# Performance work log

Hardware: AMD Instinct MI355X
Metric: run time of the kernel (lower is better)

Reference implementation:

```python
import jax, jax.numpy as jnp
import numpy as np
from jax.ops import segment_sum

N = 50000        # nodes
E = 800000       # edges (avg degree 16)
H = 128          # hidden_dim
N_ITER = 2       # BCRefinement n_iterations
TIE_P = 0.05     # fraction of tie (boundary) edges


def setup_inputs() -> dict:
    key = jax.random.key(0)
    ks = jax.random.split(key, 24)
    s = 0.02
    inp = {
        'h': jax.random.normal(ks[0], (N, H), jnp.float32),
        'e': jax.random.normal(ks[1], (E, H), jnp.float32),
        'edge_attr_raw': jax.random.normal(ks[2], (E, 10), jnp.float32),
        # edge_refine: Linear(3H,2H) -> ReLU -> Linear(2H,H)
        'W_er1': s * jax.random.normal(ks[3], (3 * H, 2 * H), jnp.float32),
        'b_er1': jnp.zeros((2 * H,), jnp.float32),
        'W_er2': s * jax.random.normal(ks[4], (2 * H, H), jnp.float32),
        'b_er2': jnp.zeros((H,), jnp.float32),
        # GRUCell(H,H) torch layout: [3H, H] chunks (r, z, n)
        'W_ih': s * jax.random.normal(ks[5], (3 * H, H), jnp.float32),
        'W_hh': s * jax.random.normal(ks[6], (3 * H, H), jnp.float32),
        'b_ih': jnp.zeros((3 * H,), jnp.float32),
        'b_hh': jnp.zeros((3 * H,), jnp.float32),
        # node_neigh_fc: Linear(H,H)
        'W_nn': s * jax.random.normal(ks[7], (H, H), jnp.float32),
        'b_nn': jnp.zeros((H,), jnp.float32),
        # gate_mlp: Linear(3H,H) -> ReLU -> Linear(H,1), last bias init -2.0
        'W_g1': s * jax.random.normal(ks[8], (3 * H, H), jnp.float32),
        'b_g1': jnp.zeros((H,), jnp.float32),
        'W_g2': s * jax.random.normal(ks[9], (H, 1), jnp.float32),
        'b_g2': jnp.full((1,), -2.0, jnp.float32),
        'edge_index': jax.random.randint(ks[10], (2, E), 0, N, jnp.int32),
        'is_tie': jax.random.uniform(ks[11], (E,)) < TIE_P,
    }
    return inp


def reference(h, e, edge_attr_raw,
              W_er1, b_er1, W_er2, b_er2,
              W_ih, W_hh, b_ih, b_hh,
              W_nn, b_nn,
              W_g1, b_g1, W_g2, b_g2,
              edge_index, is_tie):
    row = edge_index[0]
    col = edge_index[1]
    tie_f = is_tie.astype(h.dtype)                        # [E]
    internal = ~is_tie

    # coupling buses: endpoints of any tie edge (tie-incidence count > 0)
    cpl_cnt = segment_sum(tie_f, row, num_segments=N) + \
              segment_sum(tie_f, col, num_segments=N)     # [N]
    is_cpl = cpl_cnt > 0

    # internal edges pointing into coupling buses; b_smooth weights w = 1/sqrt(X^2+eps)
    to_cpl = internal & is_cpl[col]
    X = jnp.abs(edge_attr_raw[:, 1])
    w = jnp.where(to_cpl, 1.0 / jnp.sqrt(X * X + 1e-6), 0.0)
    w_den = segment_sum(w, col, num_segments=N)           # [N]
    w_norm = w / (w_den[col] + 1e-6)                      # [E], zero off-mask

    deg = jnp.maximum(cpl_cnt, 1.0)                       # clamp_min(1.0)

    h_work, e_work = h, e
    for _ in range(N_ITER):
        # --- tie-edge refinement (applied only on tie edges) ---
        edge_in = jnp.concatenate([e_work, h_work[row], h_work[col]], axis=-1)  # [E,3H]
        e_ref = jax.nn.relu(edge_in @ W_er1 + b_er1) @ W_er2 + b_er2            # [E,H]
        e_work = e_work + tie_f[:, None] * e_ref

        # --- node messages from internal neighbors into coupling buses ---
        m_node_msg = h_work[row] @ W_nn + b_nn                                   # [E,H]
        m_node_all = segment_sum(m_node_msg * w_norm[:, None], col,
                                 num_segments=N)                                 # [N,H]

        # --- mean of incident tie-edge features at each node ---
        tie_e = tie_f[:, None] * e_work                                          # [E,H]
        m_edge_all = (segment_sum(tie_e, row, num_segments=N) +
                      segment_sum(tie_e, col, num_segments=N)) / deg[:, None]    # [N,H]

        # --- gating + GRU update on coupling buses ---
        gate_in = jnp.concatenate([m_edge_all, m_node_all, h_work], axis=-1)     # [N,3H]
        gate = jax.nn.sigmoid(jax.nn.relu(gate_in @ W_g1 + b_g1) @ W_g2 + b_g2)  # [N,1]
        m = m_edge_all + gate * m_node_all                                       # [N,H]

        gi = m @ W_ih.T + b_ih                                                   # [N,3H]
        gh = h_work @ W_hh.T + b_hh
        r = jax.nn.sigmoid(gi[:, :H] + gh[:, :H])
        z = jax.nn.sigmoid(gi[:, H:2 * H] + gh[:, H:2 * H])
        n = jnp.tanh(gi[:, 2 * H:] + r * gh[:, 2 * H:])
        h_new = (1.0 - z) * n + z * h_work

        h_work = jnp.where(is_cpl[:, None], h_new, h_work)
    return h_work, e_work
```

## Files before the change

kernel.cpp:

```cpp
#include <hip/hip_runtime.h>
#include <cstdint>

#define N_NODES 50000
#define N_EDGES 800000
#define HDIM    128
#define TIE_CAP 44000
#define NITER   2
#define SCAN_B  256
#define EB_CONST 3125
#define TB_CONST 172
#define GM_T     344
#define COPY_B   1664

typedef __attribute__((ext_vector_type(8))) short bf16x8;
typedef __attribute__((ext_vector_type(4))) float f32x4;

__device__ __forceinline__ uint32_t f2bf(float f) {
    uint32_t u = __builtin_bit_cast(uint32_t, f);
    return (u + 0x7fffu + ((u >> 16) & 1u)) >> 16;
}
__device__ __forceinline__ float bf2f(uint32_t b) {
    return __builtin_bit_cast(float, b << 16);
}
__device__ __forceinline__ uint32_t comb2(uint32_t me, uint32_t mn, float g) {
    float a0 = bf2f(me & 0xffffu) + g * bf2f(mn & 0xffffu);
    float a1 = bf2f(me >> 16)     + g * bf2f(mn >> 16);
    return f2bf(a0) | (f2bf(a1) << 16);
}


__device__ __forceinline__ void stage_a128(const float* __restrict__ base,
                                           const int* __restrict__ gidx,
                                           int m0, int Mlim, char* tile, int tid)
{
    const int c = tid & 15;
    #pragma unroll
    for (int p = 0; p < 4; ++p) {
        int row = p * 32 + (tid >> 4);
        int ar = m0 + row; if (ar >= Mlim) ar = Mlim - 1;
        long g = gidx ? gidx[ar] : ar;
        const float* s = base + g * HDIM + c * 4;
        float4 v0 = *(const float4*)s;
        float4 v1 = *(const float4*)(s + 64);
        uint2 w0 = make_uint2(f2bf(v0.x) | (f2bf(v0.y) << 16),
                              f2bf(v0.z) | (f2bf(v0.w) << 16));
        uint2 w1 = make_uint2(f2bf(v1.x) | (f2bf(v1.y) << 16),
                              f2bf(v1.z) | (f2bf(v1.w) << 16));
        int sw = (row & 7) << 4;
        *(uint2*)(tile + row * 256 + ((c * 8) ^ sw)) = w0;
        *(uint2*)(tile + row * 256 + ((c * 8 + 128) ^ sw)) = w1;
    }
}

__device__ __forceinline__ void stage_bf128(const uint16_t* __restrict__ base,
                                            const int* __restrict__ gidx,
                                            int m0, int Mlim, char* tile, int tid)
{
    const int c = tid & 15;
    #pragma unroll
    for (int p = 0; p < 4; ++p) {
        int row = p * 32 + (tid >> 4);
        int ar = m0 + row; if (ar >= Mlim) ar = Mlim - 1;
        long g = gidx ? gidx[ar] : ar;
        uint4 v = *(const uint4*)(base + g * HDIM + c * 8);
        *(uint4*)(tile + row * 256 + ((c * 16) ^ ((row & 7) << 4))) = v;
    }
}

__device__ __forceinline__ void stage_b128(const short* __restrict__ BT, int ldk,
                                           int n0, int k0, char* tile, int tid)
{
    const int c = tid & 15;
    #pragma unroll
    for (int p = 0; p < 4; ++p) {
        int n = p * 32 + (tid >> 4);
        uint4 v = *(const uint4*)&BT[(size_t)(n0 + n) * ldk + k0 + c * 8];
        *(uint4*)(tile + n * 256 + ((c * 16) ^ ((n & 7) << 4))) = v;
    }
}

__device__ __forceinline__ void mfma128(const char* At, const char* Bt,
                                        int wr, int wc, int lane, f32x4 acc[4][2])
{
    #pragma unroll
    for (int ks = 0; ks < 4; ++ks) {
        int kb = ks * 64 + (lane >> 4) * 16;
        bf16x8 aF[4], bF[2];
        #pragma unroll
        for (int mi = 0; mi < 4; ++mi) {
            int row = wr * 64 + mi * 16 + (lane & 15);
            aF[mi] = *(const bf16x8*)(At + row * 256 + (kb ^ ((row & 7) << 4)));
        }
        #pragma unroll
        for (int ni = 0; ni < 2; ++ni) {
            int n = wc * 32 + ni * 16 + (lane & 15);
            bF[ni] = *(const bf16x8*)(Bt + n * 256 + (kb ^ ((n & 7) << 4)));
        }
        #pragma unroll
        for (int mi = 0; mi < 4; ++mi)
            #pragma unroll
            for (int ni = 0; ni < 2; ++ni)
                acc[mi][ni] = __builtin_amdgcn_mfma_f32_16x16x32_bf16(
                    aF[mi], bF[ni], acc[mi][ni], 0, 0, 0);
    }
}

__global__ __launch_bounds__(512)
void k_tie_fused(const float* __restrict__ e_src, float* __restrict__ out_e,
                 const float* __restrict__ e_orig,
                 const void* __restrict__ tie_raw, const int* __restrict__ counters,
                 const uint16_t* __restrict__ h_bf,
                 const int* __restrict__ tie_list, const int* __restrict__ tie_row,
                 const int* __restrict__ tie_col,
                 const short* __restrict__ BTer1, const short* __restrict__ BTer2,
                 const float* __restrict__ b_er1, const float* __restrict__ b_er2)
{
    const int tid = threadIdx.x;

    if ((int)blockIdx.x >= GM_T) {
        int fmt = counters[0];
        const float4* src = (const float4*)e_orig;
        float4* dst = (float4*)out_e;
        for (int i = ((int)blockIdx.x - GM_T) * 512 + tid;
             i < N_EDGES * (HDIM / 4); i += COPY_B * 512) {
            int row = i >> 5;
            bool t = fmt ? (((const uint8_t*)tie_raw)[row] != 0)
                         : (((const int*)tie_raw)[row] != 0);
            if (!t) dst[i] = src[i];
        }
        return;
    }

    int cnt = counters[1]; if (cnt > TIE_CAP) cnt = TIE_CAP;
    const int m0 = blockIdx.x * 128;
    if (m0 >= cnt) return;

    __shared__ __align__(16) char At[32 * 1024];
    __shared__ __align__(16) char B0[32 * 1024];
    __shared__ __align__(16) char B1[32 * 1024];

    const int lane = tid & 63;
    const int wid = tid >> 6, wr = wid >> 2, wc = wid & 3;

    f32x4 acc0[4][2] = {}, acc1[4][2] = {};
    #pragma unroll 1
    for (int c = 0; c < 3; ++c) {
        if (c == 0) stage_a128(e_src, tie_list, m0, cnt, At, tid);
        else        stage_bf128(h_bf, (c == 1) ? tie_row : tie_col, m0, cnt, At, tid);
        stage_b128(BTer1, 384, 0,   c * 128, B0, tid);
        stage_b128(BTer1, 384, 128, c * 128, B1, tid);
        __syncthreads();
        mfma128(At, B0, wr, wc, lane, acc0);
        mfma128(At, B1, wr, wc, lane, acc1);
        __syncthreads();
    }

    #pragma unroll
    for (int half = 0; half < 2; ++half) {
        char* Ct = half ? B0 : At;
        #pragma unroll
        for (int ni = 0; ni < 2; ++ni) {
            int col = wc * 32 + ni * 16 + (lane & 15);
            float bv = b_er1[half * 128 + col];
            #pragma unroll
            for (int mi = 0; mi < 4; ++mi)
                #pragma unroll
                for (int j = 0; j < 4; ++j) {
                    int rl = wr * 64 + mi * 16 + ((lane >> 4) << 2) + j;
                    float v = fmaxf((half ? acc1 : acc0)[mi][ni][j] + bv, 0.f);
                    *(uint16_t*)(Ct + rl * 256 + ((col * 2) ^ ((rl & 7) << 4))) =
                        (uint16_t)f2bf(v);
                }
        }
    }
    stage_b128(BTer2, 256, 0, 0, B1, tid);
    __syncthreads();
    f32x4 acc2[4][2] = {};
    mfma128(At, B1, wr, wc, lane, acc2);
    __syncthreads();
    stage_b128(BTer2, 256, 0, 128, B1, tid);
    __syncthreads();
    mfma128(B0, B1, wr, wc, lane, acc2);

    int col0 = wc * 32 + (lane & 15);
    float bv0 = b_er2[col0], bv1 = b_er2[col0 + 16];
    #pragma unroll
    for (int mi = 0; mi < 4; ++mi) {
        #pragma unroll
        for (int j = 0; j < 4; ++j) {
            int i = m0 + wr * 64 + mi * 16 + ((lane >> 4) << 2) + j;
            if (i < cnt) {
                int e = tie_list[i];
                #pragma unroll
                for (int ni = 0; ni < 2; ++ni) {
                    int col = col0 + ni * 16;
                    size_t eb = (size_t)e * HDIM + col;
                    out_e[eb] = e_src[eb] + acc2[mi][ni][j] + (ni ? bv1 : bv0);
                }
            }
        }
    }
}

__global__ __launch_bounds__(256)
void k_gather(const int* __restrict__ row_ptr, const int* __restrict__ csr_row,
              const float* __restrict__ csr_w, const uint16_t* __restrict__ h_bf,
              uint16_t* __restrict__ agg,
              const int* __restrict__ row_ptr2, const int* __restrict__ tcsr,
              const float* __restrict__ out_e, const float* __restrict__ deg_inv,
              uint16_t* __restrict__ m_edge_bf)
{
    int n = blockIdx.x * 4 + (threadIdx.x >> 6);
    if (n >= N_NODES) return;
    int lane = threadIdx.x & 63;

    int s = row_ptr[n], t = row_ptr[n + 1];
    float a0 = 0.f, a1 = 0.f;
    for (int j = s; j < t; ++j) {
        int r = csr_row[j];
        float w = csr_w[j];
        uint32_t v = *(const uint32_t*)(h_bf + (size_t)r * HDIM + lane * 2);
        a0 += w * bf2f(v & 0xffffu);
        a1 += w * bf2f(v >> 16);
    }
    *(uint32_t*)(agg + (size_t)n * HDIM + lane * 2) = f2bf(a0) | (f2bf(a1) << 16);

    int s2 = row_ptr2[n], t2 = row_ptr2[n + 1];
    float b0 = 0.f, b1 = 0.f;
    for (int j = s2; j < t2; ++j) {
        int e = tcsr[j];
        float2 v = *(const float2*)(out_e + (size_t)e * HDIM + lane * 2);
        b0 += v.x; b1 += v.y;
    }
    float di = deg_inv[n];
    *(uint32_t*)(m_edge_bf + (size_t)n * HDIM + lane * 2) =
        f2bf(b0 * di) | (f2bf(b1 * di) << 16);
}

__global__ __launch_bounds__(512)
void k_node_mega(const uint16_t* __restrict__ m_edge_bf,
                 const uint16_t* __restrict__ agg,
                 float* __restrict__ out_h, uint16_t* __restrict__ h_bf,
                 const float* __restrict__ cpl_cnt, const float* __restrict__ sumw,
                 const short* __restrict__ BTnn, const float* __restrict__ b_nn,
                 const short* __restrict__ BTg1, const float* __restrict__ b_g1,
                 const float* __restrict__ Wg2, const float* __restrict__ b_g2,
                 const short* __restrict__ BTcomb,
                 const short* __restrict__ BTihn, const short* __restrict__ BThhn,
                 const float* __restrict__ b_ih, const float* __restrict__ b_hh)
{
    const int m0 = blockIdx.x * 128;
    __shared__ __align__(16) char Tme[32 * 1024];
    __shared__ __align__(16) char Tmn[32 * 1024];
    __shared__ __align__(16) char Th [32 * 1024];
    __shared__ __align__(16) char Bt [32 * 1024];
    __shared__ float g_red[4][128];
    __shared__ float g_fin[128];
    __shared__ float sw_s[128];

    const int tid = threadIdx.x, lane = tid & 63;
    const int wid = tid >> 6, wr = wid >> 2, wc = wid & 3;

    stage_bf128(m_edge_bf, nullptr, m0, N_NODES, Tme, tid);
    stage_bf128(agg,       nullptr, m0, N_NODES, Tmn, tid);
    stage_bf128(h_bf,      nullptr, m0, N_NODES, Th,  tid);
    stage_b128(BTnn, 128, 0, 0, Bt, tid);
    if (tid < 128) {
        int n = m0 + tid; if (n >= N_NODES) n = N_NODES - 1;
        sw_s[tid] = sumw[n];
    }
    __syncthreads();

    {
        f32x4 accM[4][2] = {};
        mfma128(Tmn, Bt, wr, wc, lane, accM);
        __syncthreads();
        #pragma unroll
        for (int ni = 0; ni < 2; ++ni) {
            int col = wc * 32 + ni * 16 + (lane & 15);
            float bv = b_nn[col];
            #pragma unroll
            for (int mi = 0; mi < 4; ++mi)
                #pragma unroll
                for (int j = 0; j < 4; ++j) {
                    int rl = wr * 64 + mi * 16 + ((lane >> 4) << 2) + j;
                    float v = accM[mi][ni][j] + sw_s[rl] * bv;
                    *(uint16_t*)(Tmn + rl * 256 + ((col * 2) ^ ((rl & 7) << 4))) =
                        (uint16_t)f2bf(v);
                }
        }
        __syncthreads();
    }

    f32x4 accG[4][2] = {};
    #pragma unroll 1
    for (int c = 0; c < 3; ++c) {
        const char* Ac = (c == 0) ? Tme : (c == 1) ? Tmn : Th;
        stage_b128(BTg1, 384, 0, c * 128, Bt, tid);
        __syncthreads();
        mfma128(Ac, Bt, wr, wc, lane, accG);
        __syncthreads();
    }
    {
        float bg[2], wg[2];
        #pragma unroll
        for (int ni = 0; ni < 2; ++ni) {
            int col = wc * 32 + ni * 16 + (lane & 15);
            bg[ni] = b_g1[col]; wg[ni] = Wg2[col];
        }
        #pragma unroll
        for (int mi = 0; mi < 4; ++mi)
            #pragma unroll
            for (int j = 0; j < 4; ++j) {
                float p = fmaxf(accG[mi][0][j] + bg[0], 0.f) * wg[0]
                        + fmaxf(accG[mi][1][j] + bg[1], 0.f) * wg[1];
                #pragma unroll
                for (int o = 8; o; o >>= 1) p += __shfl_xor(p, o);
                if ((lane & 15) == 0)
                    g_red[wc][wr * 64 + mi * 16 + ((lane >> 4) << 2) + j] = p;
            }
    }
    __syncthreads();
    if (tid < 128) {
        float t = g_red[0][tid] + g_red[1][tid] + g_red[2][tid] + g_red[3][tid]
                + b_g2[0];
        g_fin[tid] = 1.f / (1.f + __expf(-t));
    }
    __syncthreads();

    stage_b128(BTcomb, 256, 0, 0, Bt, tid);
    {
        const int c = tid & 15;
        #pragma unroll
        for (int p = 0; p < 4; ++p) {
            int row = p * 32 + (tid >> 4);
            float g = g_fin[row];
            int sw = (row & 7) << 4;
            #pragma unroll
            for (int hh = 0; hh < 2; ++hh) {
                int off = (c * 8 + hh * 128) ^ sw;
                uint2 me2 = *(uint2*)(Tme + row * 256 + off);
                uint2 mn2 = *(uint2*)(Tmn + row * 256 + off);
                *(uint2*)(Tmn + row * 256 + off) =
                    make_uint2(comb2(me2.x, mn2.x, g), comb2(me2.y, mn2.y, g));
            }
        }
    }
    __syncthreads();

    f32x4 aR[4][2] = {}, aZ[4][2] = {}, aGI[4][2] = {}, aGH[4][2] = {};
    stage_b128(BTcomb, 256, 0, 128, Tme, tid);
    mfma128(Tmn, Bt, wr, wc, lane, aR);   __syncthreads();
    stage_b128(BTcomb, 256, 128, 0, Bt, tid);
    mfma128(Th, Tme, wr, wc, lane, aR);   __syncthreads();
    stage_b128(BTcomb, 256, 128, 128, Tme, tid);
    mfma128(Tmn, Bt, wr, wc, lane, aZ);   __syncthreads();
    stage_b128(BTihn, 128, 0, 0, Bt, tid);
    mfma128(Th, Tme, wr, wc, lane, aZ);   __syncthreads();
    stage_b128(BThhn, 128, 0, 0, Tme, tid);
    mfma128(Tmn, Bt, wr, wc, lane, aGI);  __syncthreads();
    mfma128(Th, Tme, wr, wc, lane, aGH);

    #pragma unroll
    for (int ni = 0; ni < 2; ++ni) {
        int col = wc * 32 + ni * 16 + (lane & 15);
        float br  = b_ih[col] + b_hh[col];
        float bz  = b_ih[128 + col] + b_hh[128 + col];
        float bin = b_ih[256 + col], bhn = b_hh[256 + col];
        #pragma unroll
        for (int mi = 0; mi < 4; ++mi)
            #pragma unroll
            for (int j = 0; j < 4; ++j) {
                int node = m0 + wr * 64 + mi * 16 + ((lane >> 4) << 2) + j;
                if (node < N_NODES && cpl_cnt[node] > 0.f) {
                    float r = 1.f / (1.f + __expf(-(aR[mi][ni][j] + br)));
                    float z = 1.f / (1.f + __expf(-(aZ[mi][ni][j] + bz)));
                    float nn = tanhf(aGI[mi][ni][j] + bin + r * (aGH[mi][ni][j] + bhn));
                    size_t hb = (size_t)node * HDIM + col;
                    float hv = out_h[hb];
                    float hn = (1.f - z) * nn + z * hv;
                    out_h[hb] = hn;
                    h_bf[hb] = (uint16_t)f2bf(hn);
                }
            }
    }
}

#define INIT_BLOCKS 449

__global__ __launch_bounds__(256)
void k_init(const float* __restrict__ h, float* __restrict__ out_h,
            uint16_t* __restrict__ h_bf,
            float* __restrict__ cpl_cnt, float* __restrict__ w_den,
            int* __restrict__ hist, int* __restrict__ counters,
            const uint8_t* __restrict__ tie_raw,
            const float* __restrict__ W_er1, const float* __restrict__ W_er2,
            const float* __restrict__ W_nn, const float* __restrict__ W_g1,
            const float* __restrict__ W_ih, const float* __restrict__ W_hh,
            short* __restrict__ BTer1, short* __restrict__ BTer2,
            short* __restrict__ BTnn, short* __restrict__ BTg1,
            short* __restrict__ BTcomb, short* __restrict__ BTihn,
            short* __restrict__ BThhn)
{
    const int b = blockIdx.x, t = threadIdx.x;
    if (b < 256) {
        for (int i = b * 256 + t; i < N_NODES * HDIM / 4; i += 256 * 256) {
            float4 v = ((const float4*)h)[i];
            ((float4*)out_h)[i] = v;
            *(uint2*)(h_bf + (size_t)i * 4) =
                make_uint2(f2bf(v.x) | (f2bf(v.y) << 16),
                           f2bf(v.z) | (f2bf(v.w) << 16));
        }
    } else if (b < 320) {
        for (int i = (b - 256) * 256 + t; i < N_NODES; i += 64 * 256) {
            cpl_cnt[i] = 0.f; w_den[i] = 0.f; hist[i] = 0;
        }
    } else if (b < 448) {
        for (int i = (b - 320) * 256 + t; i < 384 * 256; i += 128 * 256) {
            {   int n = i / 384, k = i % 384;
                BTer1[i] = (short)f2bf(W_er1[(size_t)k * 256 + n]); }
            if (i < 128 * 256) {
                int n = i / 256, k = i % 256;
                BTer2[i] = (short)f2bf(W_er2[(size_t)k * 128 + n]); }
            if (i < 128 * 128) {
                int n = i / 128, k = i % 128;
                BTnn[i] = (short)f2bf(W_nn[(size_t)k * 128 + n]); }
            if (i < 128 * 384) {
                int n = i / 384, k = i % 384;
                BTg1[i] = (short)f2bf(W_g1[(size_t)k * 128 + n]); }
            if (i < 256 * 256) {
                int n = i >> 8, k = i & 255;
                float v = (k < 128) ? W_ih[n * 128 + k] : W_hh[n * 128 + (k - 128)];
                BTcomb[i] = (short)f2bf(v); }
            if (i < 128 * 128) {
                BTihn[i] = (short)f2bf(W_ih[256 * 128 + i]);
                BThhn[i] = (short)f2bf(W_hh[256 * 128 + i]); }
        }
    } else {
        if (t < 64) {
            int c = 0;
            for (int k = t; k < 4096; k += 64)
                if ((k & 3) && tie_raw[k]) c = 1;
            unsigned long long m = __ballot(c != 0);
            if (t == 0) {
                counters[0] = (m != 0ull) ? 1 : 0;
                counters[1] = 0; counters[2] = 0; counters[3] = 0;
            }
        }
    }
}

__global__ __launch_bounds__(256)
void k_tie(const void* __restrict__ tie_raw, const int* __restrict__ counters,
           const int* __restrict__ ei, float* __restrict__ cpl_cnt,
           int* __restrict__ tie_cnt, int* __restrict__ tie_list,
           int* __restrict__ tie_row, int* __restrict__ tie_col)
{
    int e = blockIdx.x * 256 + threadIdx.x;
    int fmt = counters[0];
    bool t = false; int r = 0, c = 0;
    if (e < N_EDGES)
        t = fmt ? (((const uint8_t*)tie_raw)[e] != 0)
                : (((const int*)tie_raw)[e] != 0);
    if (t) {
        r = ei[e]; c = ei[N_EDGES + e];
        atomicAdd(&cpl_cnt[r], 1.f);
        atomicAdd(&cpl_cnt[c], 1.f);
    }
    unsigned long long m = __ballot(t);
    if (m == 0ull) return;
    int lane = threadIdx.x & 63;
    int first = __ffsll((unsigned long long)m) - 1;
    int base = 0;
    if (lane == first) base = atomicAdd(tie_cnt, __popcll(m));
    base = __shfl(base, first);
    if (t) {
        int idx = base + __popcll(m & ((1ull << lane) - 1ull));
        if (idx < TIE_CAP) { tie_list[idx] = e; tie_row[idx] = r; tie_col[idx] = c; }
    }
}

__global__ __launch_bounds__(256)
void k_w(const void* __restrict__ tie_raw, const int* __restrict__ counters,
         const int* __restrict__ ei, const float* __restrict__ attr,
         const float* __restrict__ cpl_cnt, float* __restrict__ w_den,
         float* __restrict__ w_arr, int* __restrict__ hist)
{
    int e = blockIdx.x * 256 + threadIdx.x;
    if (e >= N_EDGES) return;
    int fmt = counters[0];
    bool t = fmt ? (((const uint8_t*)tie_raw)[e] != 0)
                 : (((const int*)tie_raw)[e] != 0);
    float w = 0.f;
    if (!t) {
        int c = ei[N_EDGES + e];
        if (cpl_cnt[c] > 0.f) {
            float X = fabsf(attr[(size_t)e * 10 + 1]);
            w = 1.f / sqrtf(X * X + 1e-6f);
            atomicAdd(&w_den[c], w);
            atomicAdd(&hist[c], 1);
        }
    }
    w_arr[e] = w;
}

__global__ __launch_bounds__(SCAN_B)
void k_scan1(const int* __restrict__ hist, const float* __restrict__ cpl_cnt,
             int* __restrict__ excl, int* __restrict__ bsum,
             int* __restrict__ excl2, int* __restrict__ bsum2)
{
    __shared__ int s[SCAN_B];
    int t = threadIdx.x;
    int i = blockIdx.x * SCAN_B + t;
    int v = (i < N_NODES) ? hist[i] : 0;
    s[t] = v;
    __syncthreads();
    for (int o = 1; o < SCAN_B; o <<= 1) {
        int u = (t >= o) ? s[t - o] : 0;
        __syncthreads();
        s[t] += u;
        __syncthreads();
    }
    if (i < N_NODES) excl[i] = s[t] - v;
    if (t == SCAN_B - 1) bsum[blockIdx.x] = s[t];
    __syncthreads();
    int v2 = (i < N_NODES) ? (int)cpl_cnt[i] : 0;
    s[t] = v2;
    __syncthreads();
    for (int o = 1; o < SCAN_B; o <<= 1) {
        int u = (t >= o) ? s[t - o] : 0;
        __syncthreads();
        s[t] += u;
        __syncthreads();
    }
    if (i < N_NODES) excl2[i] = s[t] - v2;
    if (t == SCAN_B - 1) bsum2[blockIdx.x] = s[t];
}

__global__ void k_scan2(int* __restrict__ bsum, int* __restrict__ bsum2,
                        int* __restrict__ counters)
{
    const int NB = (N_NODES + SCAN_B - 1) / SCAN_B;
    if (threadIdx.x == 0) {
        int run = 0;
        for (int b = 0; b < NB; ++b) { int x = bsum[b]; bsum[b] = run; run += x; }
        counters[2] = run;
        int run2 = 0;
        for (int b = 0; b < NB; ++b) { int x = bsum2[b]; bsum2[b] = run2; run2 += x; }
        counters[3] = run2;
    }
}

__global__ __launch_bounds__(256)
void k_scan3(const int* __restrict__ excl, const int* __restrict__ bsum,
             const int* __restrict__ excl2, const int* __restrict__ bsum2,
             int* __restrict__ row_ptr, int* __restrict__ cursor,
             int* __restrict__ row_ptr2, int* __restrict__ cursor2,
             const int* __restrict__ counters,
             const float* __restrict__ cpl_cnt, const float* __restrict__ w_den,
             float* __restrict__ deg_inv, float* __restrict__ sumw)
{
    int i = blockIdx.x * 256 + threadIdx.x;
    if (i < N_NODES) {
        int v = excl[i] + bsum[i >> 8];
        row_ptr[i] = v;  cursor[i] = v;
        int v2 = excl2[i] + bsum2[i >> 8];
        row_ptr2[i] = v2; cursor2[i] = v2;
        deg_inv[i] = 1.f / fmaxf(cpl_cnt[i], 1.f);
        float wd = w_den[i];
        sumw[i] = wd / (wd + 1e-6f);
    }
    if (i == N_NODES) {
        row_ptr[N_NODES] = counters[2];
        row_ptr2[N_NODES] = counters[3];
    }
}

__global__ __launch_bounds__(256)
void k_fill(const int* __restrict__ ei, const float* __restrict__ w_arr,
            const float* __restrict__ w_den, int* __restrict__ cursor,
            int* __restrict__ csr_row, float* __restrict__ csr_w,
            const int* __restrict__ counters, const int* __restrict__ tie_list,
            const int* __restrict__ tie_row, const int* __restrict__ tie_col,
            int* __restrict__ cursor2, int* __restrict__ tcsr)
{
    int b = blockIdx.x;
    if (b < EB_CONST) {
        int e = b * 256 + threadIdx.x;
        if (e >= N_EDGES) return;
        float w = w_arr[e];
        if (w == 0.f) return;
        int c = ei[N_EDGES + e];
        int pos = atomicAdd(&cursor[c], 1);
        csr_row[pos] = ei[e];
        csr_w[pos] = w / (w_den[c] + 1e-6f);
    } else {
        int i = (b - EB_CONST) * 256 + threadIdx.x;
        int cnt = counters[1]; if (cnt > TIE_CAP) cnt = TIE_CAP;
        if (i < cnt) {
            int e = tie_list[i];
            int p1 = atomicAdd(&cursor2[tie_row[i]], 1); tcsr[p1] = e;
            int p2 = atomicAdd(&cursor2[tie_col[i]], 1); tcsr[p2] = e;
        }
    }
}

extern "C" void kernel_launch(void* const* d_in, const int* in_sizes, int n_in,
                              void* d_out, int out_size, void* d_ws, size_t ws_size,
                              hipStream_t stream)
{
    const float* h     = (const float*)d_in[0];
    const float* e     = (const float*)d_in[1];
    const float* attr  = (const float*)d_in[2];
    const float* W_er1 = (const float*)d_in[3];
    const float* b_er1 = (const float*)d_in[4];
    const float* W_er2 = (const float*)d_in[5];
    const float* b_er2 = (const float*)d_in[6];
    const float* W_ih  = (const float*)d_in[7];
    const float* W_hh  = (const float*)d_in[8];
    const float* b_ih  = (const float*)d_in[9];
    const float* b_hh  = (const float*)d_in[10];
    const float* W_nn  = (const float*)d_in[11];
    const float* b_nn  = (const float*)d_in[12];
    const float* W_g1  = (const float*)d_in[13];
    const float* b_g1  = (const float*)d_in[14];
    const float* W_g2  = (const float*)d_in[15];
    const float* b_g2  = (const float*)d_in[16];
    const int*   ei    = (const int*)d_in[17];
    const void*  tie_raw = d_in[18];

    float* out_h = (float*)d_out;
    float* out_e = out_h + (size_t)N_NODES * HDIM;

    char* ws = (char*)d_ws;
    size_t off = 0;
    auto alloc = [&](size_t bytes) -> void* {
        void* p = ws + off;
        off = (off + bytes + 255) & ~(size_t)255;
        return p;
    };
    float* cpl_cnt = (float*)alloc((size_t)N_NODES * 4);
    float* w_den   = (float*)alloc((size_t)N_NODES * 4);
    int*   hist    = (int*)  alloc((size_t)N_NODES * 4);
    int*   counters= (int*)  alloc(256);
    float* deg_inv = (float*)alloc((size_t)N_NODES * 4);
    float* sumw    = (float*)alloc((size_t)N_NODES * 4);
    float* w_arr   = (float*)alloc((size_t)N_EDGES * 4);
    int* tie_list  = (int*)alloc((size_t)TIE_CAP * 4);
    int* tie_row   = (int*)alloc((size_t)TIE_CAP * 4);
    int* tie_col   = (int*)alloc((size_t)TIE_CAP * 4);
    short* BTer1   = (short*)alloc((size_t)256 * 384 * 2);
    short* BTer2   = (short*)alloc((size_t)128 * 256 * 2);
    short* BTnn    = (short*)alloc((size_t)128 * 128 * 2);
    short* BTg1    = (short*)alloc((size_t)128 * 384 * 2);
    short* BTcomb  = (short*)alloc((size_t)256 * 256 * 2);
    short* BTihn   = (short*)alloc((size_t)128 * 128 * 2);
    short* BThhn   = (short*)alloc((size_t)128 * 128 * 2);
    uint16_t* h_bf = (uint16_t*)alloc((size_t)N_NODES * HDIM * 2);
    uint16_t* agg  = (uint16_t*)alloc((size_t)N_NODES * HDIM * 2);
    uint16_t* m_edge_bf = (uint16_t*)alloc((size_t)N_NODES * HDIM * 2);
    int* excl      = (int*)alloc((size_t)N_NODES * 4);
    int* excl2     = (int*)alloc((size_t)N_NODES * 4);
    int* bsum      = (int*)alloc(256 * 4);
    int* bsum2     = (int*)alloc(256 * 4);
    int* row_ptr   = (int*)alloc((size_t)(N_NODES + 1) * 4);
    int* row_ptr2  = (int*)alloc((size_t)(N_NODES + 1) * 4);
    int* cursor    = (int*)alloc((size_t)N_NODES * 4);
    int* cursor2   = (int*)alloc((size_t)N_NODES * 4);
    int* csr_row   = (int*)alloc((size_t)N_EDGES * 4);
    float* csr_w   = (float*)alloc((size_t)N_EDGES * 4);
    int* tcsr      = (int*)alloc((size_t)2 * TIE_CAP * 4);
    if (off > ws_size) return;

    const int GM_N = (N_NODES + 127) / 128;
    const int NB   = (N_NODES + SCAN_B - 1) / SCAN_B;

    k_init<<<INIT_BLOCKS, 256, 0, stream>>>(
        h, out_h, h_bf, cpl_cnt, w_den, hist, counters,
        (const uint8_t*)tie_raw,
        W_er1, W_er2, W_nn, W_g1, W_ih, W_hh,
        BTer1, BTer2, BTnn, BTg1, BTcomb, BTihn, BThhn);
    k_tie<<<EB_CONST, 256, 0, stream>>>(tie_raw, counters, ei, cpl_cnt,
                                        counters + 1, tie_list, tie_row, tie_col);
    k_w<<<EB_CONST, 256, 0, stream>>>(tie_raw, counters, ei, attr, cpl_cnt,
                                      w_den, w_arr, hist);
    k_scan1<<<NB, SCAN_B, 0, stream>>>(hist, cpl_cnt, excl, bsum, excl2, bsum2);
    k_scan2<<<1, 64, 0, stream>>>(bsum, bsum2, counters);
    k_scan3<<<(N_NODES + 256) / 256, 256, 0, stream>>>(
        excl, bsum, excl2, bsum2, row_ptr, cursor, row_ptr2, cursor2,
        counters, cpl_cnt, w_den, deg_inv, sumw);
    k_fill<<<EB_CONST + TB_CONST, 256, 0, stream>>>(
        ei, w_arr, w_den, cursor, csr_row, csr_w,
        counters, tie_list, tie_row, tie_col, cursor2, tcsr);

    for (int it = 0; it < NITER; ++it) {
        const float* e_src = (it == 0) ? e : out_e;
        int grid = (it == 0) ? (GM_T + COPY_B) : GM_T;
        k_tie_fused<<<grid, 512, 0, stream>>>(
            e_src, out_e, e, tie_raw, counters, h_bf,
            tie_list, tie_row, tie_col,
            BTer1, BTer2, b_er1, b_er2);
        k_gather<<<(N_NODES + 3) / 4, 256, 0, stream>>>(
            row_ptr, csr_row, csr_w, h_bf, agg,
            row_ptr2, tcsr, out_e, deg_inv, m_edge_bf);
        k_node_mega<<<GM_N, 512, 0, stream>>>(
            m_edge_bf, agg, out_h, h_bf, cpl_cnt, sumw,
            BTnn, b_nn, BTg1, b_g1, W_g2, b_g2,
            BTcomb, BTihn, BThhn, b_ih, b_hh);
    }
}
```

Before: 979.7 us.

## Split non-tie edge copy across setup kernels to overlap with latency-bound work

The bulk copy of non-tie edge features into the output was previously done by extra blocks of the first fused tie-edge MLP kernel. It is now split into three chunks, each handled by extra blocks appended to the k_tie, k_w and k_fill setup kernels. Those kernels are atomic- and latency-bound, so the bandwidth-heavy copy is meant to fill otherwise idle memory bandwidth and shorten the first iteration. The risk is that the extra copy blocks delay the setup kernels' own critical-path work or compete with their atomics.

```diff
diff --git a/kernel.cpp b/kernel.cpp
--- a/kernel.cpp
+++ b/kernel.cpp
@@ -10,7 +10,9 @@
 #define EB_CONST 3125
 #define TB_CONST 172
 #define GM_T     344
-#define COPY_B   1664
+#define TOTQ     (N_EDGES * (HDIM / 4))
+#define CPB      555
+#define CCHUNK   ((TOTQ + 2) / 3)
 
 typedef __attribute__((ext_vector_type(8))) short bf16x8;
 typedef __attribute__((ext_vector_type(4))) float f32x4;
@@ -26,6 +28,23 @@
     float a0 = bf2f(me & 0xffffu) + g * bf2f(mn & 0xffffu);
     float a1 = bf2f(me >> 16)     + g * bf2f(mn >> 16);
     return f2bf(a0) | (f2bf(a1) << 16);
+}
+
+__device__ __forceinline__ void copy_seg(const float* __restrict__ e,
+                                         float* __restrict__ out_e,
+                                         const void* __restrict__ tie_raw, int fmt,
+                                         int cb, int tid, int seg)
+{
+    int start = seg * CCHUNK;
+    int end = start + CCHUNK; if (end > TOTQ) end = TOTQ;
+    const float4* src = (const float4*)e;
+    float4* dst = (float4*)out_e;
+    for (int i = start + cb * 256 + tid; i < end; i += CPB * 256) {
+        int row = i >> 5;
+        bool t = fmt ? (((const uint8_t*)tie_raw)[row] != 0)
+                     : (((const int*)tie_raw)[row] != 0);
+        if (!t) dst[i] = src[i];
+    }
 }
 
 
@@ -107,30 +126,13 @@
 
 __global__ __launch_bounds__(512)
 void k_tie_fused(const float* __restrict__ e_src, float* __restrict__ out_e,
-                 const float* __restrict__ e_orig,
-                 const void* __restrict__ tie_raw, const int* __restrict__ counters,
+                 const int* __restrict__ counters,
                  const uint16_t* __restrict__ h_bf,
                  const int* __restrict__ tie_list, const int* __restrict__ tie_row,
                  const int* __restrict__ tie_col,
                  const short* __restrict__ BTer1, const short* __restrict__ BTer2,
                  const float* __restrict__ b_er1, const float* __restrict__ b_er2)
 {
-    const int tid = threadIdx.x;
-
-    if ((int)blockIdx.x >= GM_T) {
-        int fmt = counters[0];
-        const float4* src = (const float4*)e_orig;
-        float4* dst = (float4*)out_e;
-        for (int i = ((int)blockIdx.x - GM_T) * 512 + tid;
-             i < N_EDGES * (HDIM / 4); i += COPY_B * 512) {
-            int row = i >> 5;
-            bool t = fmt ? (((const uint8_t*)tie_raw)[row] != 0)
-                         : (((const int*)tie_raw)[row] != 0);
-            if (!t) dst[i] = src[i];
-        }
-        return;
-    }
-
     int cnt = counters[1]; if (cnt > TIE_CAP) cnt = TIE_CAP;
     const int m0 = blockIdx.x * 128;
     if (m0 >= cnt) return;
@@ -139,7 +141,7 @@
     __shared__ __align__(16) char B0[32 * 1024];
     __shared__ __align__(16) char B1[32 * 1024];
 
-    const int lane = tid & 63;
+    const int tid = threadIdx.x, lane = tid & 63;
     const int wid = tid >> 6, wr = wid >> 2, wc = wid & 3;
 
     f32x4 acc0[4][2] = {}, acc1[4][2] = {};
@@ -454,16 +456,21 @@
 void k_tie(const void* __restrict__ tie_raw, const int* __restrict__ counters,
            const int* __restrict__ ei, float* __restrict__ cpl_cnt,
            int* __restrict__ tie_cnt, int* __restrict__ tie_list,
-           int* __restrict__ tie_row, int* __restrict__ tie_col)
-{
-    int e = blockIdx.x * 256 + threadIdx.x;
+           int* __restrict__ tie_row, int* __restrict__ tie_col,
+           const float* __restrict__ e, float* __restrict__ out_e)
+{
     int fmt = counters[0];
+    if ((int)blockIdx.x >= EB_CONST) {
+        copy_seg(e, out_e, tie_raw, fmt, (int)blockIdx.x - EB_CONST, threadIdx.x, 0);
+        return;
+    }
+    int e_idx = blockIdx.x * 256 + threadIdx.x;
     bool t = false; int r = 0, c = 0;
-    if (e < N_EDGES)
-        t = fmt ? (((const uint8_t*)tie_raw)[e] != 0)
-                : (((const int*)tie_raw)[e] != 0);
+    if (e_idx < N_EDGES)
+        t = fmt ? (((const uint8_t*)tie_raw)[e_idx] != 0)
+                : (((const int*)tie_raw)[e_idx] != 0);
     if (t) {
-        r = ei[e]; c = ei[N_EDGES + e];
+        r = ei[e_idx]; c = ei[N_EDGES + e_idx];
         atomicAdd(&cpl_cnt[r], 1.f);
         atomicAdd(&cpl_cnt[c], 1.f);
     }
@@ -476,7 +483,7 @@
     base = __shfl(base, first);
     if (t) {
         int idx = base + __popcll(m & ((1ull << lane) - 1ull));
-        if (idx < TIE_CAP) { tie_list[idx] = e; tie_row[idx] = r; tie_col[idx] = c; }
+        if (idx < TIE_CAP) { tie_list[idx] = e_idx; tie_row[idx] = r; tie_col[idx] = c; }
     }
 }
 
@@ -484,24 +491,29 @@
 void k_w(const void* __restrict__ tie_raw, const int* __restrict__ counters,
          const int* __restrict__ ei, const float* __restrict__ attr,
          const float* __restrict__ cpl_cnt, float* __restrict__ w_den,
-         float* __restrict__ w_arr, int* __restrict__ hist)
-{
-    int e = blockIdx.x * 256 + threadIdx.x;
-    if (e >= N_EDGES) return;
+         float* __restrict__ w_arr, int* __restrict__ hist,
+         const float* __restrict__ e, float* __restrict__ out_e)
+{
     int fmt = counters[0];
-    bool t = fmt ? (((const uint8_t*)tie_raw)[e] != 0)
-                 : (((const int*)tie_raw)[e] != 0);
+    if ((int)blockIdx.x >= EB_CONST) {
+        copy_seg(e, out_e, tie_raw, fmt, (int)blockIdx.x - EB_CONST, threadIdx.x, 1);
+        return;
+    }
+    int e_idx = blockIdx.x * 256 + threadIdx.x;
+    if (e_idx >= N_EDGES) return;
+    bool t = fmt ? (((const uint8_t*)tie_raw)[e_idx] != 0)
+                 : (((const int*)tie_raw)[e_idx] != 0);
     float w = 0.f;
     if (!t) {
-        int c = ei[N_EDGES + e];
+        int c = ei[N_EDGES + e_idx];
         if (cpl_cnt[c] > 0.f) {
-            float X = fabsf(attr[(size_t)e * 10 + 1]);
+            float X = fabsf(attr[(size_t)e_idx * 10 + 1]);
             w = 1.f / sqrtf(X * X + 1e-6f);
             atomicAdd(&w_den[c], w);
             atomicAdd(&hist[c], 1);
         }
     }
-    w_arr[e] = w;
+    w_arr[e_idx] = w;
 }
 
 __global__ __launch_bounds__(SCAN_B)
@@ -582,25 +594,32 @@
             int* __restrict__ csr_row, float* __restrict__ csr_w,
             const int* __restrict__ counters, const int* __restrict__ tie_list,
             const int* __restrict__ tie_row, const int* __restrict__ tie_col,
-            int* __restrict__ cursor2, int* __restrict__ tcsr)
+            int* __restrict__ cursor2, int* __restrict__ tcsr,
+            const void* __restrict__ tie_raw,
+            const float* __restrict__ e, float* __restrict__ out_e)
 {
     int b = blockIdx.x;
+    if (b >= EB_CONST + TB_CONST) {
+        copy_seg(e, out_e, tie_raw, counters[0], b - (EB_CONST + TB_CONST),
+                 threadIdx.x, 2);
+        return;
+    }
     if (b < EB_CONST) {
-        int e = b * 256 + threadIdx.x;
-        if (e >= N_EDGES) return;
-        float w = w_arr[e];
+        int e_idx = b * 256 + threadIdx.x;
+        if (e_idx >= N_EDGES) return;
+        float w = w_arr[e_idx];
         if (w == 0.f) return;
-        int c = ei[N_EDGES + e];
+        int c = ei[N_EDGES + e_idx];
         int pos = atomicAdd(&cursor[c], 1);
-        csr_row[pos] = ei[e];
+        csr_row[pos] = ei[e_idx];
         csr_w[pos] = w / (w_den[c] + 1e-6f);
     } else {
         int i = (b - EB_CONST) * 256 + threadIdx.x;
         int cnt = counters[1]; if (cnt > TIE_CAP) cnt = TIE_CAP;
         if (i < cnt) {
-            int e = tie_list[i];
-            int p1 = atomicAdd(&cursor2[tie_row[i]], 1); tcsr[p1] = e;
-            int p2 = atomicAdd(&cursor2[tie_col[i]], 1); tcsr[p2] = e;
+            int e_idx = tie_list[i];
+            int p1 = atomicAdd(&cursor2[tie_row[i]], 1); tcsr[p1] = e_idx;
+            int p2 = atomicAdd(&cursor2[tie_col[i]], 1); tcsr[p2] = e_idx;
         }
     }
 }
@@ -680,25 +699,25 @@
         (const uint8_t*)tie_raw,
         W_er1, W_er2, W_nn, W_g1, W_ih, W_hh,
         BTer1, BTer2, BTnn, BTg1, BTcomb, BTihn, BThhn);
-    k_tie<<<EB_CONST, 256, 0, stream>>>(tie_raw, counters, ei, cpl_cnt,
-                                        counters + 1, tie_list, tie_row, tie_col);
-    k_w<<<EB_CONST, 256, 0, stream>>>(tie_raw, counters, ei, attr, cpl_cnt,
-                                      w_den, w_arr, hist);
+    k_tie<<<EB_CONST + CPB, 256, 0, stream>>>(
+        tie_raw, counters, ei, cpl_cnt, counters + 1,
+        tie_list, tie_row, tie_col, e, out_e);
+    k_w<<<EB_CONST + CPB, 256, 0, stream>>>(
+        tie_raw, counters, ei, attr, cpl_cnt, w_den, w_arr, hist, e, out_e);
     k_scan1<<<NB, SCAN_B, 0, stream>>>(hist, cpl_cnt, excl, bsum, excl2, bsum2);
     k_scan2<<<1, 64, 0, stream>>>(bsum, bsum2, counters);
     k_scan3<<<(N_NODES + 256) / 256, 256, 0, stream>>>(
         excl, bsum, excl2, bsum2, row_ptr, cursor, row_ptr2, cursor2,
         counters, cpl_cnt, w_den, deg_inv, sumw);
-    k_fill<<<EB_CONST + TB_CONST, 256, 0, stream>>>(
+    k_fill<<<EB_CONST + TB_CONST + CPB, 256, 0, stream>>>(
         ei, w_arr, w_den, cursor, csr_row, csr_w,
-        counters, tie_list, tie_row, tie_col, cursor2, tcsr);
+        counters, tie_list, tie_row, tie_col, cursor2, tcsr,
+        tie_raw, e, out_e);
 
     for (int it = 0; it < NITER; ++it) {
         const float* e_src = (it == 0) ? e : out_e;
-        int grid = (it == 0) ? (GM_T + COPY_B) : GM_T;
-        k_tie_fused<<<grid, 512, 0, stream>>>(
-            e_src, out_e, e, tie_raw, counters, h_bf,
-            tie_list, tie_row, tie_col,
+        k_tie_fused<<<GM_T, 512, 0, stream>>>(
+            e_src, out_e, counters, h_bf, tie_list, tie_row, tie_col,
             BTer1, BTer2, b_er1, b_er2);
         k_gather<<<(N_NODES + 3) / 4, 256, 0, stream>>>(
             row_ptr, csr_row, csr_w, h_bf, agg,
```

Result: no change. 975.0 us (-0.5%).
